# Kernel optimization log

Measured on AMD Instinct MI355X. Metric: run time of the kernel, lower is better.

## Reference

```python
import jax, jax.numpy as jnp
import numpy as np

MARGIN = 1.0


def _rand_offdiag(key, n):
    # uniform random index j != k for each row k (replaces Python random.choice)
    j = jax.random.randint(key, (n,), 0, n - 1)
    return j + (j >= jnp.arange(n)).astype(j.dtype)


def _semi_hard_margin_loss(logits, j_rand, j_fallback, margin):
    # logits: [N, N]; anchor for row k is logits[k, k]
    n = logits.shape[0]
    rows = jnp.arange(n)
    anchor = jnp.diagonal(logits)                      # [N]
    # term 1: random imposter, hinge at 0 (loss added only when diff > 0)
    imp1 = logits[rows, j_rand]
    d1 = jnp.maximum(imp1 - anchor + margin, 0.0)
    # term 2: semi-hard imposter = max over entries strictly below the anchor
    neg_inf = jnp.finfo(logits.dtype).min
    mask = logits < anchor[:, None]                    # diagonal never True
    cand_max = jnp.max(jnp.where(mask, logits, neg_inf), axis=1)
    has_cand = jnp.any(mask, axis=1)
    imp2 = jnp.where(has_cand, cand_max, logits[rows, j_fallback])
    d2 = jnp.maximum(imp2 - anchor + margin, 0.0)
    return jnp.mean(d1 + d2)


def setup_inputs() -> dict:
    key = jax.random.key(0)
    kx, ky = jax.random.split(key)
    x = jax.random.normal(kx, (4096, 1024), dtype=jnp.float32)
    y = jax.random.normal(ky, (4096, 1024), dtype=jnp.float32)
    return {"x": x, "y": y}


def reference(x, y):
    logits = jnp.matmul(x, y.T)                        # [N, N]
    n = logits.shape[0]
    k1, k2, k3, k4 = jax.random.split(jax.random.key(42), 4)
    loss = (_semi_hard_margin_loss(logits, _rand_offdiag(k1, n), _rand_offdiag(k2, n), MARGIN)
            + _semi_hard_margin_loss(logits.T, _rand_offdiag(k3, n), _rand_offdiag(k4, n), MARGIN))
    return loss
```

## Files before the change

kernel.cpp:

```cpp
#include <hip/hip_runtime.h>
#include <stdint.h>
#include <stddef.h>

#define NN 4096
#define KK 1024
#define SPAN 4095u

typedef unsigned short ushort_t;
typedef __attribute__((ext_vector_type(8))) short short8v;
typedef __attribute__((ext_vector_type(4))) float f32x4;

__host__ __device__ inline void tf2x32(uint32_t k0, uint32_t k1,
                                       uint32_t x0, uint32_t x1,
                                       uint32_t* o0, uint32_t* o1) {
  uint32_t ks2 = k0 ^ k1 ^ 0x1BD11BDAu;
  uint32_t v0 = x0 + k0;
  uint32_t v1 = x1 + k1;
#define TF_ROT(x, r) (((x) << (r)) | ((x) >> (32 - (r))))
#define TF_RND(r) do { v0 += v1; v1 = TF_ROT(v1, r); v1 ^= v0; } while (0)
  TF_RND(13); TF_RND(15); TF_RND(26); TF_RND(6);
  v0 += k1;  v1 += ks2 + 1u;
  TF_RND(17); TF_RND(29); TF_RND(16); TF_RND(24);
  v0 += ks2; v1 += k0 + 2u;
  TF_RND(13); TF_RND(15); TF_RND(26); TF_RND(6);
  v0 += k0;  v1 += k1 + 3u;
  TF_RND(17); TF_RND(29); TF_RND(16); TF_RND(24);
  v0 += k1;  v1 += ks2 + 4u;
  TF_RND(13); TF_RND(15); TF_RND(26); TF_RND(6);
  v0 += ks2; v1 += k0 + 5u;
#undef TF_RND
#undef TF_ROT
  *o0 = v0; *o1 = v1;
}

__device__ inline uint32_t rb32(uint32_t ka, uint32_t kb, uint32_t i) {
  uint32_t a, b;
  tf2x32(ka, kb, 0u, i, &a, &b);
  return a ^ b;
}

__device__ inline uint32_t fenc(float f) {
  uint32_t b = __float_as_uint(f);
  return (b & 0x80000000u) ? ~b : (b | 0x80000000u);
}
__device__ inline float fdec(uint32_t e) {
  uint32_t b = (e & 0x80000000u) ? (e & 0x7FFFFFFFu) : ~e;
  return __uint_as_float(b);
}

__device__ inline ushort_t bf16rne(float f) {
  uint32_t u = __float_as_uint(f);
  return (ushort_t)((u + 0x7FFFu + ((u >> 16) & 1u)) >> 16);
}

__device__ inline void glds16(const void* g, void* l) {
  __builtin_amdgcn_global_load_lds((const __attribute__((address_space(1))) void*)g,
                                   (__attribute__((address_space(3))) void*)l, 16, 0, 0);
}

__global__ __launch_bounds__(256) void k_prep(
    const float4* __restrict__ X, const float4* __restrict__ Y,
    ushort4* __restrict__ Xb, ushort4* __restrict__ Yb,
    uint32_t* __restrict__ rowmax, uint32_t* __restrict__ colmax) {
  const int b = blockIdx.x, tid = threadIdx.x;
  if (b < 16) rowmax[b * 256 + tid] = 0u;
  else if (b < 32) colmax[(b - 16) * 256 + tid] = 0u;
  const float4* src = (b < 2048) ? X : Y;
  ushort4* dst = (b < 2048) ? Xb : Yb;
  const int n4 = NN * KK / 4;
  for (int i = (b & 2047) * 256 + tid; i < n4; i += 2048 * 256) {
    float4 v = src[i];
    ushort4 o;
    o.x = bf16rne(v.x); o.y = bf16rne(v.y); o.z = bf16rne(v.z); o.w = bf16rne(v.w);
    dst[i] = o;
  }
}

__global__ __launch_bounds__(256) void k_dots(
    const float* __restrict__ X, const float* __restrict__ Y,
    uint32_t s0a, uint32_t s0b, uint32_t s1a, uint32_t s1b,
    uint32_t s2a, uint32_t s2b, uint32_t s3a, uint32_t s3b,
    float* __restrict__ anchor, float* __restrict__ irr, float* __restrict__ irf,
    float* __restrict__ icr, float* __restrict__ icf) {
  const int wid = threadIdx.x >> 6;
  const int lane = threadIdx.x & 63;
  const int row = blockIdx.x * 4 + wid;

  int jl = 0;
  if (lane < 4) {
    uint32_t ka = (lane == 0) ? s0a : (lane == 1) ? s1a : (lane == 2) ? s2a : s3a;
    uint32_t kb = (lane == 0) ? s0b : (lane == 1) ? s1b : (lane == 2) ? s2b : s3b;
    uint32_t k1a, k1b, k2a, k2b;
    tf2x32(ka, kb, 0u, 0u, &k1a, &k1b);
    tf2x32(ka, kb, 0u, 1u, &k2a, &k2b);
    uint32_t hi = rb32(k1a, k1b, (uint32_t)row);
    uint32_t lo = rb32(k2a, k2b, (uint32_t)row);
    uint32_t off = ((hi % SPAN) * 256u + (lo % SPAN)) % SPAN;
    int j = (int)off;
    jl = j + ((j >= row) ? 1 : 0);
  }
  const int j1r = __shfl(jl, 0), j1f = __shfl(jl, 1);
  const int j2r = __shfl(jl, 2), j2f = __shfl(jl, 3);

  const float4* xk = (const float4*)(X + (size_t)row * KK);
  const float4* yk = (const float4*)(Y + (size_t)row * KK);
  const float4* y1 = (const float4*)(Y + (size_t)j1r * KK);
  const float4* y2 = (const float4*)(Y + (size_t)j1f * KK);
  const float4* x1 = (const float4*)(X + (size_t)j2r * KK);
  const float4* x2 = (const float4*)(X + (size_t)j2f * KK);
  float sa = 0.f, s1 = 0.f, s2 = 0.f, s3 = 0.f, s4 = 0.f;
  for (int t = lane; t < KK / 4; t += 64) {
    float4 xv = xk[t], yv = yk[t], a1 = y1[t], a2 = y2[t], b1 = x1[t], b2 = x2[t];
    sa = fmaf(xv.x, yv.x, fmaf(xv.y, yv.y, fmaf(xv.z, yv.z, fmaf(xv.w, yv.w, sa))));
    s1 = fmaf(xv.x, a1.x, fmaf(xv.y, a1.y, fmaf(xv.z, a1.z, fmaf(xv.w, a1.w, s1))));
    s2 = fmaf(xv.x, a2.x, fmaf(xv.y, a2.y, fmaf(xv.z, a2.z, fmaf(xv.w, a2.w, s2))));
    s3 = fmaf(b1.x, yv.x, fmaf(b1.y, yv.y, fmaf(b1.z, yv.z, fmaf(b1.w, yv.w, s3))));
    s4 = fmaf(b2.x, yv.x, fmaf(b2.y, yv.y, fmaf(b2.z, yv.z, fmaf(b2.w, yv.w, s4))));
  }
  for (int m = 32; m >= 1; m >>= 1) {
    sa += __shfl_xor(sa, m);
    s1 += __shfl_xor(s1, m);
    s2 += __shfl_xor(s2, m);
    s3 += __shfl_xor(s3, m);
    s4 += __shfl_xor(s4, m);
  }
  if (lane == 0) {
    anchor[row] = sa; irr[row] = s1; irf[row] = s2; icr[row] = s3; icf[row] = s4;
  }
}


__global__ __launch_bounds__(512, 2) void k_gemm256(
    const ushort_t* __restrict__ A, const ushort_t* __restrict__ B,
    const float* __restrict__ anchor,
    uint32_t* __restrict__ rowmax, uint32_t* __restrict__ colmax) {
  __shared__ ushort_t AL[2][256 * 64];
  __shared__ ushort_t BL[2][256 * 64];

  const int tid = threadIdx.x;
  const int lane = tid & 63;
  const int w = tid >> 6, wr = w >> 2, wc = w & 3;
  const int l15 = lane & 15, l4 = lane >> 4;

  const int swz = (blockIdx.x & 7) * 32 + (blockIdx.x >> 3);
  const int bi = swz >> 4, bj = swz & 15;

  const int strow = tid >> 3;
  const int scol = ((tid & 7) ^ (strow & 7)) * 8;
  const ushort_t* Asrc = A + (size_t)(bi * 256 + strow) * KK + scol;
  const ushort_t* Bsrc = B + (size_t)(bj * 256 + strow) * KK + scol;

  const int arow0 = wr * 128 + l15;
  const int brow0 = wc * 64 + l15;
  const int ap0 = ((l4) ^ (l15 & 7)) * 8;
  const int ap1 = ((4 + l4) ^ (l15 & 7)) * 8;

  f32x4 acc[8][4] = {};

#define MFMA16(a, b, c) __builtin_amdgcn_mfma_f32_16x16x32_bf16(a, b, c, 0, 0, 0)

#pragma unroll
  for (int i = 0; i < 4; ++i)
    glds16(Asrc + (size_t)i * 64 * KK, &AL[0][tid * 8 + i * 4096]);
#pragma unroll
  for (int i = 0; i < 4; ++i)
    glds16(Bsrc + (size_t)i * 64 * KK, &BL[0][tid * 8 + i * 4096]);
  __syncthreads();

  for (int t = 0; t < 16; ++t) {
    const int buf = t & 1, nxt = buf ^ 1;
    const size_t kk = (size_t)(t + 1) * 64;
    short8v af[8], b0, b1;

    if (t < 15) {
#pragma unroll
      for (int i = 0; i < 4; ++i)
        glds16(Asrc + (size_t)i * 64 * KK + kk, &AL[nxt][tid * 8 + i * 4096]);
    }
#pragma unroll
    for (int m = 0; m < 8; ++m)
      af[m] = *(const short8v*)&AL[buf][(arow0 + m * 16) * 64 + ap0];
    b0 = *(const short8v*)&BL[buf][(brow0) * 64 + ap0];
    b1 = *(const short8v*)&BL[buf][(brow0 + 16) * 64 + ap0];
    __builtin_amdgcn_s_setprio(1);
#pragma unroll
    for (int m = 0; m < 8; ++m) {
      acc[m][0] = MFMA16(af[m], b0, acc[m][0]);
      acc[m][1] = MFMA16(af[m], b1, acc[m][1]);
    }
    __builtin_amdgcn_s_setprio(0);

    if (t < 15) {
#pragma unroll
      for (int i = 0; i < 4; ++i)
        glds16(Bsrc + (size_t)i * 64 * KK + kk, &BL[nxt][tid * 8 + i * 4096]);
    }
    b0 = *(const short8v*)&BL[buf][(brow0 + 32) * 64 + ap0];
    b1 = *(const short8v*)&BL[buf][(brow0 + 48) * 64 + ap0];
    __builtin_amdgcn_s_setprio(1);
#pragma unroll
    for (int m = 0; m < 8; ++m) {
      acc[m][2] = MFMA16(af[m], b0, acc[m][2]);
      acc[m][3] = MFMA16(af[m], b1, acc[m][3]);
    }
    __builtin_amdgcn_s_setprio(0);

#pragma unroll
    for (int m = 0; m < 8; ++m)
      af[m] = *(const short8v*)&AL[buf][(arow0 + m * 16) * 64 + ap1];
    b0 = *(const short8v*)&BL[buf][(brow0) * 64 + ap1];
    b1 = *(const short8v*)&BL[buf][(brow0 + 16) * 64 + ap1];
    __builtin_amdgcn_s_setprio(1);
#pragma unroll
    for (int m = 0; m < 8; ++m) {
      acc[m][0] = MFMA16(af[m], b0, acc[m][0]);
      acc[m][1] = MFMA16(af[m], b1, acc[m][1]);
    }
    __builtin_amdgcn_s_setprio(0);

    b0 = *(const short8v*)&BL[buf][(brow0 + 32) * 64 + ap1];
    b1 = *(const short8v*)&BL[buf][(brow0 + 48) * 64 + ap1];
    __builtin_amdgcn_s_setprio(1);
#pragma unroll
    for (int m = 0; m < 8; ++m) {
      acc[m][2] = MFMA16(af[m], b0, acc[m][2]);
      acc[m][3] = MFMA16(af[m], b1, acc[m][3]);
    }
    __builtin_amdgcn_s_setprio(0);

    __syncthreads();
  }
#undef MFMA16

  const int rbase = bi * 256 + wr * 128;
  const int cbase = bj * 256 + wc * 64;

  float ar[32], ac[4];
#pragma unroll
  for (int m = 0; m < 8; ++m)
#pragma unroll
    for (int r = 0; r < 4; ++r)
      ar[m * 4 + r] = anchor[rbase + m * 16 + l4 * 4 + r];
#pragma unroll
  for (int n = 0; n < 4; ++n)
    ac[n] = anchor[cbase + n * 16 + l15];

#pragma unroll
  for (int m = 0; m < 8; ++m) {
#pragma unroll
    for (int r = 0; r < 4; ++r) {
      const int rg = rbase + m * 16 + l4 * 4 + r;
      const float a = ar[m * 4 + r];
      uint32_t e = 0;
#pragma unroll
      for (int n = 0; n < 4; ++n) {
        const int cg = cbase + n * 16 + l15;
        float v = acc[m][n][r];
        if (v < a && rg != cg) { uint32_t fe = fenc(v); e = (fe > e) ? fe : e; }
      }
#pragma unroll
      for (int sh = 1; sh < 16; sh <<= 1) {
        uint32_t o = (uint32_t)__shfl_xor((int)e, sh, 64);
        e = (o > e) ? o : e;
      }
      if (l15 == 0 && e) atomicMax(&rowmax[rg], e);
    }
  }
#pragma unroll
  for (int n = 0; n < 4; ++n) {
    const int cg = cbase + n * 16 + l15;
    const float a = ac[n];
    uint32_t e = 0;
#pragma unroll
    for (int m = 0; m < 8; ++m) {
#pragma unroll
      for (int r = 0; r < 4; ++r) {
        const int rg = rbase + m * 16 + l4 * 4 + r;
        float v = acc[m][n][r];
        if (v < a && rg != cg) { uint32_t fe = fenc(v); e = (fe > e) ? fe : e; }
      }
    }
    {
      uint32_t o = (uint32_t)__shfl_xor((int)e, 16, 64); e = (o > e) ? o : e;
      o = (uint32_t)__shfl_xor((int)e, 32, 64);          e = (o > e) ? o : e;
    }
    if (l4 == 0 && e) atomicMax(&colmax[cg], e);
  }
}

__global__ __launch_bounds__(256) void k_final(
    const float* __restrict__ anchor,
    const float* __restrict__ irr, const float* __restrict__ irf,
    const float* __restrict__ icr, const float* __restrict__ icf,
    const uint32_t* __restrict__ rowmax, const uint32_t* __restrict__ colmax,
    float* __restrict__ out) {
  float s = 0.f;
  for (int k = (int)threadIdx.x; k < NN; k += 256) {
    float a = anchor[k];
    float d1 = fmaxf(irr[k] - a + 1.0f, 0.f);
    uint32_t rm = rowmax[k];
    float imp2r = rm ? fdec(rm) : irf[k];
    float d2 = fmaxf(imp2r - a + 1.0f, 0.f);
    float e1 = fmaxf(icr[k] - a + 1.0f, 0.f);
    uint32_t cm = colmax[k];
    float imp2c = cm ? fdec(cm) : icf[k];
    float e2 = fmaxf(imp2c - a + 1.0f, 0.f);
    s += d1 + d2 + e1 + e2;
  }
  __shared__ float red[4];
  for (int m = 32; m >= 1; m >>= 1) s += __shfl_xor(s, m);
  if ((threadIdx.x & 63) == 0) red[threadIdx.x >> 6] = s;
  __syncthreads();
  if (threadIdx.x == 0) out[0] = (red[0] + red[1] + red[2] + red[3]) * (1.0f / NN);
}

extern "C" void kernel_launch(void* const* d_in, const int* in_sizes, int n_in,
                              void* d_out, int out_size, void* d_ws, size_t ws_size,
                              hipStream_t stream) {
  const float* X = (const float*)d_in[0];
  const float* Y = (const float*)d_in[1];
  float* out = (float*)d_out;

  char* ws = (char*)d_ws;
  float* anchor    = (float*)(ws + 0 * 16384);
  float* irr       = (float*)(ws + 1 * 16384);
  float* irf       = (float*)(ws + 2 * 16384);
  float* icr       = (float*)(ws + 3 * 16384);
  float* icf       = (float*)(ws + 4 * 16384);
  uint32_t* rowmax = (uint32_t*)(ws + 5 * 16384);
  uint32_t* colmax = (uint32_t*)(ws + 6 * 16384);
  ushort_t* Xb     = (ushort_t*)(ws + 256 * 1024);
  ushort_t* Yb     = Xb + (size_t)NN * KK;

  uint32_t sk[4][2];
  for (int i = 0; i < 4; ++i) tf2x32(0u, 42u, 0u, (uint32_t)i, &sk[i][0], &sk[i][1]);

  k_prep<<<4096, 256, 0, stream>>>((const float4*)X, (const float4*)Y,
                                   (ushort4*)Xb, (ushort4*)Yb, rowmax, colmax);

  k_dots<<<NN / 4, 256, 0, stream>>>(X, Y,
      sk[0][0], sk[0][1], sk[1][0], sk[1][1], sk[2][0], sk[2][1], sk[3][0], sk[3][1],
      anchor, irr, irf, icr, icf);

  k_gemm256<<<256, 512, 0, stream>>>(Xb, Yb, anchor, rowmax, colmax);

  k_final<<<1, 256, 0, stream>>>(anchor, irr, irf, icr, icf, rowmax, colmax, out);
}
```

Measured before the change: 99.88 us.

## Restructure GEMM main loop into 8-phase ping-pong schedule with explicit waitcnt barriers

Replaces the double-buffered k-loop of the 256x256 bf16 GEMM with an 8-phase schedule per pair of k-tiles. Each phase does LDS fragment loads, an MFMA cluster and staged global-to-LDS loads, separated by explicit s_barrier, lgkmcnt and vmcnt waits plus sched_barriers. It also splits the LDS tiles into halves and reorders the MFMA k-halves within each cluster. The aim is to overlap global loads, LDS reads and MFMA work more tightly, at the cost of many more barriers. The wrapped tail prefetch (kt & 15) reloads tiles into buffers that are never consumed afterward.

```diff
diff --git a/kernel.cpp b/kernel.cpp
--- a/kernel.cpp
+++ b/kernel.cpp
@@ -130,12 +130,12 @@
 }
 
 
-__global__ __launch_bounds__(512, 2) void k_gemm256(
+__global__ __launch_bounds__(512, 2) void k_gemm8p(
     const ushort_t* __restrict__ A, const ushort_t* __restrict__ B,
     const float* __restrict__ anchor,
     uint32_t* __restrict__ rowmax, uint32_t* __restrict__ colmax) {
-  __shared__ ushort_t AL[2][256 * 64];
-  __shared__ ushort_t BL[2][256 * 64];
+  __shared__ ushort_t AL[2][2][8192];
+  __shared__ ushort_t BL[2][2][8192];
 
   const int tid = threadIdx.x;
   const int lane = tid & 63;
@@ -147,90 +147,127 @@
 
   const int strow = tid >> 3;
   const int scol = ((tid & 7) ^ (strow & 7)) * 8;
-  const ushort_t* Asrc = A + (size_t)(bi * 256 + strow) * KK + scol;
-  const ushort_t* Bsrc = B + (size_t)(bj * 256 + strow) * KK + scol;
-
-  const int arow0 = wr * 128 + l15;
-  const int brow0 = wc * 64 + l15;
-  const int ap0 = ((l4) ^ (l15 & 7)) * 8;
-  const int ap1 = ((4 + l4) ^ (l15 & 7)) * 8;
+  const ushort_t* Abase = A + (size_t)(bi * 256 + strow) * KK + scol;
+  const ushort_t* Bbase = B + (size_t)(bj * 256 + strow) * KK + scol;
+
+  const int ss0 = ((0 * 4 + l4) ^ (l15 & 7)) * 8;
+  const int ss1 = ((1 * 4 + l4) ^ (l15 & 7)) * 8;
+  const int bhalf = wc >> 1, brow0 = (wc & 1) * 64 + l15;
 
   f32x4 acc[8][4] = {};
-
-#define MFMA16(a, b, c) __builtin_amdgcn_mfma_f32_16x16x32_bf16(a, b, c, 0, 0, 0)
-
-#pragma unroll
-  for (int i = 0; i < 4; ++i)
-    glds16(Asrc + (size_t)i * 64 * KK, &AL[0][tid * 8 + i * 4096]);
-#pragma unroll
-  for (int i = 0; i < 4; ++i)
-    glds16(Bsrc + (size_t)i * 64 * KK, &BL[0][tid * 8 + i * 4096]);
-  __syncthreads();
-
-  for (int t = 0; t < 16; ++t) {
-    const int buf = t & 1, nxt = buf ^ 1;
-    const size_t kk = (size_t)(t + 1) * 64;
-    short8v af[8], b0, b1;
-
-    if (t < 15) {
-#pragma unroll
-      for (int i = 0; i < 4; ++i)
-        glds16(Asrc + (size_t)i * 64 * KK + kk, &AL[nxt][tid * 8 + i * 4096]);
-    }
-#pragma unroll
-    for (int m = 0; m < 8; ++m)
-      af[m] = *(const short8v*)&AL[buf][(arow0 + m * 16) * 64 + ap0];
-    b0 = *(const short8v*)&BL[buf][(brow0) * 64 + ap0];
-    b1 = *(const short8v*)&BL[buf][(brow0 + 16) * 64 + ap0];
-    __builtin_amdgcn_s_setprio(1);
-#pragma unroll
-    for (int m = 0; m < 8; ++m) {
-      acc[m][0] = MFMA16(af[m], b0, acc[m][0]);
-      acc[m][1] = MFMA16(af[m], b1, acc[m][1]);
-    }
-    __builtin_amdgcn_s_setprio(0);
-
-    if (t < 15) {
-#pragma unroll
-      for (int i = 0; i < 4; ++i)
-        glds16(Bsrc + (size_t)i * 64 * KK + kk, &BL[nxt][tid * 8 + i * 4096]);
-    }
-    b0 = *(const short8v*)&BL[buf][(brow0 + 32) * 64 + ap0];
-    b1 = *(const short8v*)&BL[buf][(brow0 + 48) * 64 + ap0];
-    __builtin_amdgcn_s_setprio(1);
-#pragma unroll
-    for (int m = 0; m < 8; ++m) {
-      acc[m][2] = MFMA16(af[m], b0, acc[m][2]);
-      acc[m][3] = MFMA16(af[m], b1, acc[m][3]);
-    }
-    __builtin_amdgcn_s_setprio(0);
-
-#pragma unroll
-    for (int m = 0; m < 8; ++m)
-      af[m] = *(const short8v*)&AL[buf][(arow0 + m * 16) * 64 + ap1];
-    b0 = *(const short8v*)&BL[buf][(brow0) * 64 + ap1];
-    b1 = *(const short8v*)&BL[buf][(brow0 + 16) * 64 + ap1];
-    __builtin_amdgcn_s_setprio(1);
-#pragma unroll
-    for (int m = 0; m < 8; ++m) {
-      acc[m][0] = MFMA16(af[m], b0, acc[m][0]);
-      acc[m][1] = MFMA16(af[m], b1, acc[m][1]);
-    }
-    __builtin_amdgcn_s_setprio(0);
-
-    b0 = *(const short8v*)&BL[buf][(brow0 + 32) * 64 + ap1];
-    b1 = *(const short8v*)&BL[buf][(brow0 + 48) * 64 + ap1];
-    __builtin_amdgcn_s_setprio(1);
-#pragma unroll
-    for (int m = 0; m < 8; ++m) {
-      acc[m][2] = MFMA16(af[m], b0, acc[m][2]);
-      acc[m][3] = MFMA16(af[m], b1, acc[m][3]);
-    }
-    __builtin_amdgcn_s_setprio(0);
-
-    __syncthreads();
-  }
-#undef MFMA16
+  short8v Areg[4][2], B0r[2][2], B1r[2][2];
+
+#define STAGE_A(DD, KT)                                                        \
+  do {                                                                         \
+    glds16(Abase + (size_t)0 * KK + (KT) * 64,   &AL[DD][0][tid * 8]);         \
+    glds16(Abase + (size_t)64 * KK + (KT) * 64,  &AL[DD][0][4096 + tid * 8]);  \
+    glds16(Abase + (size_t)128 * KK + (KT) * 64, &AL[DD][1][tid * 8]);         \
+    glds16(Abase + (size_t)192 * KK + (KT) * 64, &AL[DD][1][4096 + tid * 8]);  \
+  } while (0)
+#define STAGE_B(DD, KT)                                                        \
+  do {                                                                         \
+    glds16(Bbase + (size_t)0 * KK + (KT) * 64,   &BL[DD][0][tid * 8]);         \
+    glds16(Bbase + (size_t)64 * KK + (KT) * 64,  &BL[DD][0][4096 + tid * 8]);  \
+    glds16(Bbase + (size_t)128 * KK + (KT) * 64, &BL[DD][1][tid * 8]);         \
+    glds16(Bbase + (size_t)192 * KK + (KT) * 64, &BL[DD][1][4096 + tid * 8]);  \
+  } while (0)
+
+#define BAR() do { __builtin_amdgcn_s_barrier(); \
+                   __builtin_amdgcn_sched_barrier(0); } while (0)
+#define LGKM0() do { asm volatile("s_waitcnt lgkmcnt(0)" ::: "memory"); \
+                     __builtin_amdgcn_sched_barrier(0); } while (0)
+#define VM8BAR() do { asm volatile("s_waitcnt vmcnt(8)" ::: "memory"); \
+                      __builtin_amdgcn_s_barrier(); \
+                      __builtin_amdgcn_sched_barrier(0); } while (0)
+
+#define MFMA1(a, b, c) c = __builtin_amdgcn_mfma_f32_16x16x32_bf16(a, b, c, 0, 0, 0)
+#define CL16(MS, NS, BR)                                                       \
+  do {                                                                         \
+    __builtin_amdgcn_s_setprio(1);                                             \
+    _Pragma("unroll")                                                          \
+    for (int q = 0; q < 4; ++q) {                                              \
+      MFMA1(Areg[q][0], BR[0][0], acc[(MS) * 4 + q][(NS) * 2]);                \
+      MFMA1(Areg[q][0], BR[1][0], acc[(MS) * 4 + q][(NS) * 2 + 1]);            \
+      MFMA1(Areg[q][1], BR[0][1], acc[(MS) * 4 + q][(NS) * 2]);                \
+      MFMA1(Areg[q][1], BR[1][1], acc[(MS) * 4 + q][(NS) * 2 + 1]);            \
+    }                                                                          \
+    __builtin_amdgcn_s_setprio(0);                                             \
+  } while (0)
+
+#define LDA(D, M, KH) (*(const short8v*)&AL[D][wr][((M) * 16 + l15) * 64 + ((KH) ? ss1 : ss0)])
+#define LDB(D, N, KH) (*(const short8v*)&BL[D][bhalf][(brow0 + (N) * 16) * 64 + ((KH) ? ss1 : ss0)])
+
+  STAGE_B(0, 0); STAGE_A(0, 0);
+  STAGE_B(1, 1); STAGE_A(1, 1);
+  asm volatile("s_waitcnt vmcnt(8)" ::: "memory");
+  __builtin_amdgcn_s_barrier();
+  __builtin_amdgcn_sched_barrier(0);
+
+  for (int i = 0; i < 8; ++i) {
+    const int kt2 = (2 * i + 2) & 15, kt3 = (2 * i + 3) & 15;
+
+#pragma unroll
+    for (int q = 0; q < 4; ++q) { Areg[q][0] = LDA(0, q, 0); Areg[q][1] = LDA(0, q, 1); }
+#pragma unroll
+    for (int n = 0; n < 2; ++n) { B0r[n][0] = LDB(0, n, 0); B0r[n][1] = LDB(0, n, 1); }
+    BAR(); LGKM0();
+    CL16(0, 0, B0r);
+    BAR();
+
+#pragma unroll
+    for (int n = 0; n < 2; ++n) { B1r[n][0] = LDB(0, n + 2, 0); B1r[n][1] = LDB(0, n + 2, 1); }
+    BAR(); LGKM0();
+    CL16(0, 1, B1r);
+    BAR();
+
+#pragma unroll
+    for (int q = 0; q < 4; ++q) { Areg[q][0] = LDA(0, q + 4, 0); Areg[q][1] = LDA(0, q + 4, 1); }
+    STAGE_B(0, kt2);
+    BAR(); LGKM0();
+    CL16(1, 1, B1r);
+    BAR();
+
+    STAGE_A(0, kt2);
+    BAR(); LGKM0();
+    CL16(1, 0, B0r);
+    VM8BAR();
+
+#pragma unroll
+    for (int q = 0; q < 4; ++q) { Areg[q][0] = LDA(1, q, 0); Areg[q][1] = LDA(1, q, 1); }
+#pragma unroll
+    for (int n = 0; n < 2; ++n) { B0r[n][0] = LDB(1, n, 0); B0r[n][1] = LDB(1, n, 1); }
+    BAR(); LGKM0();
+    CL16(0, 0, B0r);
+    BAR();
+
+#pragma unroll
+    for (int n = 0; n < 2; ++n) { B1r[n][0] = LDB(1, n + 2, 0); B1r[n][1] = LDB(1, n + 2, 1); }
+    BAR(); LGKM0();
+    CL16(0, 1, B1r);
+    BAR();
+
+#pragma unroll
+    for (int q = 0; q < 4; ++q) { Areg[q][0] = LDA(1, q + 4, 0); Areg[q][1] = LDA(1, q + 4, 1); }
+    STAGE_B(1, kt3);
+    BAR(); LGKM0();
+    CL16(1, 1, B1r);
+    BAR();
+
+    STAGE_A(1, kt3);
+    BAR(); LGKM0();
+    CL16(1, 0, B0r);
+    VM8BAR();
+  }
+
+#undef LDA
+#undef LDB
+#undef CL16
+#undef MFMA1
+#undef VM8BAR
+#undef LGKM0
+#undef BAR
+#undef STAGE_A
+#undef STAGE_B
 
   const int rbase = bi * 256 + wr * 128;
   const int cbase = bj * 256 + wc * 64;
@@ -342,7 +379,7 @@
       sk[0][0], sk[0][1], sk[1][0], sk[1][1], sk[2][0], sk[2][1], sk[3][0], sk[3][1],
       anchor, irr, irf, icr, icf);
 
-  k_gemm256<<<256, 512, 0, stream>>>(Xb, Yb, anchor, rowmax, colmax);
+  k_gemm8p<<<256, 512, 0, stream>>>(Xb, Yb, anchor, rowmax, colmax);
 
   k_final<<<1, 256, 0, stream>>>(anchor, irr, irf, icr, icf, rowmax, colmax, out);
 }
```

New measurement: 94.77 us. -5.1%, faster.
